# Optimization experiments

Measured on AMD Instinct MI355X. Metric: run time of the kernel, lower is better.

## Reference

```python
import jax, jax.numpy as jnp
import numpy as np

B, S, D, H = 4, 1024, 1024, 16
DK = D // H
MASK_WEIGHT_0 = 1.0   # weight for key-type 0 (from (weight, mask_mat) tuple)
MASK_WEIGHT_1 = 0.5   # weight for key-type 1
NEG_INF = -1.0e9


def setup_inputs() -> dict:
    key = jax.random.key(0)
    ks = jax.random.split(key, 10)
    wscale = 0.02
    return {
        "query": jax.random.normal(ks[0], (B, S, D), jnp.float32),
        "key_x": jax.random.normal(ks[1], (B, S, D), jnp.float32),
        "value": jax.random.normal(ks[2], (B, S, D), jnp.float32),
        "mask0": jax.random.randint(ks[3], (B, S, S), 0, 2, jnp.int32),
        "mask1": jax.random.randint(ks[4], (B, S, S), 0, 2, jnp.int32),
        "Wq":  wscale * jax.random.normal(ks[5], (D, D), jnp.float32),
        "Wk0": wscale * jax.random.normal(ks[6], (D, D), jnp.float32),
        "Wk1": wscale * jax.random.normal(ks[7], (D, D), jnp.float32),
        "Wv":  wscale * jax.random.normal(ks[8], (D, D), jnp.float32),
        "Wo":  wscale * jax.random.normal(ks[9], (D, D), jnp.float32),
    }


def _heads(x, W):
    # torch nn.Linear: x @ W.T ; then view(B,S,H,DK).transpose(1,2)
    return (x @ W.T).reshape(B, S, H, DK).transpose(0, 2, 1, 3)  # [B,H,S,DK]


def reference(query, key_x, value, mask0, mask1, Wq, Wk0, Wk1, Wv, Wo):
    q = _heads(query, Wq)          # [B,H,S,DK]
    k0 = _heads(key_x, Wk0)
    k1 = _heads(key_x, Wk1)
    v = _heads(value, Wv)
    scale = 1.0 / jnp.sqrt(jnp.float32(DK))

    def masked_score(k, mask, weight):
        s = jnp.einsum('bhqd,bhkd->bhqk', q, k) * scale       # [B,H,S,S]
        keep = (mask != 0)[:, None, :, :]                     # broadcast over heads
        # (score * weight*keep).masked_fill(mask==0, -1e9)
        return jnp.where(keep, s * weight, NEG_INF)

    scores = masked_score(k0, mask0, MASK_WEIGHT_0) + masked_score(k1, mask1, MASK_WEIGHT_1)
    p_attn = jax.nn.sigmoid(scores)                           # activation='sigmoid'
    x = jnp.einsum('bhqk,bhkd->bhqd', p_attn, v)              # [B,H,S,DK]
    x = x.transpose(0, 2, 1, 3).reshape(B, S, D)
    return x @ Wo.T                                            # output_linear (dropout p=0)
```

## Files before the change

kernel.cpp:

```cpp
#include <hip/hip_runtime.h>

#define B_  4
#define S_  1024
#define D_  1024
#define H_  16
#define DK_ 64

typedef __attribute__((ext_vector_type(8)))  short bf16x8;
typedef __attribute__((ext_vector_type(4)))  short bf16x4;
typedef __attribute__((ext_vector_type(4)))  float f32x4;
typedef __attribute__((ext_vector_type(16))) float f32x16;

static __device__ __forceinline__ unsigned short f2bf(float f) {
  union { float f; unsigned u; } v; v.f = f;
  unsigned r = v.u + 0x7FFFu + ((v.u >> 16) & 1u);
  return (unsigned short)(r >> 16);
}

static __device__ __forceinline__ unsigned cvtpk(float lo, float hi) {
  unsigned r;
  asm("v_cvt_pk_bf16_f32 %0, %1, %2" : "=v"(r) : "v"(lo), "v"(hi));
  return r;
}
static __device__ __forceinline__ void plswap(unsigned &a, unsigned &b) {
  asm volatile("v_permlane32_swap_b32 %0, %1" : "+v"(a), "+v"(b));
}

typedef __attribute__((address_space(1))) const void gc_t;
typedef __attribute__((address_space(3))) void lds_t;
static __device__ __forceinline__ void gload_lds16(const void* g, void* l) {
  __builtin_amdgcn_global_load_lds((gc_t*)g, (lds_t*)l, 16, 0, 0);
}

#define TM_ (1u << 22)
#define WM_ (1u << 20)

#define CEXP_ (-0.18033688011112042f)

__global__ __launch_bounds__(256)
void cvt_w(const float* __restrict__ w0, const float* __restrict__ w1,
           const float* __restrict__ w2, const float* __restrict__ w3,
           const float* __restrict__ w4, unsigned short* __restrict__ wbf)
{
  const size_t u = ((size_t)blockIdx.x * 256 + threadIdx.x) * 8;
  const int seg = (int)(u >> 20);
  const size_t off = u & (WM_ - 1);
  unsigned short t[8];
  if (seg == 1) {
    float4 a0 = *(const float4*)(w1 + off);
    float4 a1 = *(const float4*)(w1 + off + 4);
    float4 b0 = *(const float4*)(w2 + off);
    float4 b1 = *(const float4*)(w2 + off + 4);
    t[0]=f2bf(a0.x+0.5f*b0.x); t[1]=f2bf(a0.y+0.5f*b0.y);
    t[2]=f2bf(a0.z+0.5f*b0.z); t[3]=f2bf(a0.w+0.5f*b0.w);
    t[4]=f2bf(a1.x+0.5f*b1.x); t[5]=f2bf(a1.y+0.5f*b1.y);
    t[6]=f2bf(a1.z+0.5f*b1.z); t[7]=f2bf(a1.w+0.5f*b1.w);
  } else {
    const float sc = (seg == 0) ? CEXP_ : 1.0f;
    const float* src = (seg == 0) ? w0 : (seg == 2 ? w3 : w4);
    float4 f0 = *(const float4*)(src + off);
    float4 f1 = *(const float4*)(src + off + 4);
    t[0]=f2bf(sc*f0.x); t[1]=f2bf(sc*f0.y);
    t[2]=f2bf(sc*f0.z); t[3]=f2bf(sc*f0.w);
    t[4]=f2bf(sc*f1.x); t[5]=f2bf(sc*f1.y);
    t[6]=f2bf(sc*f1.z); t[7]=f2bf(sc*f1.w);
  }
  *(bf16x8*)(wbf + (size_t)seg * WM_ + off) = *(bf16x8*)t;
}

__global__ __launch_bounds__(256, 4)
void proj_gemm(const float* __restrict__ qx, const float* __restrict__ kx,
               const float* __restrict__ vx,
               const unsigned short* __restrict__ wbf,
               unsigned short* __restrict__ Qb, unsigned short* __restrict__ Kh,
               unsigned short* __restrict__ Vth,
               const int* __restrict__ ma, const int* __restrict__ mb,
               unsigned long long* __restrict__ pk)
{
  __shared__ unsigned short As[128][64];
  __shared__ unsigned short Ws[128][64];

  const int tid = threadIdx.x, bid = blockIdx.x;

  if (bid >= 768) {
    const int row = bid - 768;
    const int w4  = tid >> 6, lw = tid & 63;
    const int4 a  = *(const int4*)(ma + (size_t)row*1024 + w4*256 + lw*4);
    const int4 b  = *(const int4*)(mb + (size_t)row*1024 + w4*256 + lw*4);
    const unsigned long long b0 = __ballot((a.x != 0) & (b.x != 0));
    const unsigned long long b1 = __ballot((a.y != 0) & (b.y != 0));
    const unsigned long long b2 = __ballot((a.z != 0) & (b.z != 0));
    const unsigned long long b3 = __ballot((a.w != 0) & (b.w != 0));
    if (lw < 4) {
      const unsigned long long wv =
            ((b0 >> (16*lw)) & 0xFFFFull)
         | (((b1 >> (16*lw)) & 0xFFFFull) << 16)
         | (((b2 >> (16*lw)) & 0xFFFFull) << 32)
         | (((b3 >> (16*lw)) & 0xFFFFull) << 48);
      pk[(size_t)row*16 + w4*4 + lw] = wv;
    }
    return;
  }

  const int xcd = bid & 7, c = bid >> 3;
  const int L = xcd * 96 + c;
  const int which = L >> 8;
  const int rem = L & 255;
  const int mt = rem >> 3, nt = rem & 7;
  const int m0 = mt * 128, n0 = nt * 128;
  const int w = tid >> 6, l = tid & 63;
  const int lr = l & 15, lg = l >> 4;
  const int wr = w >> 1, wc = w & 1;

  const float* Af = (which == 0) ? qx : (which == 1) ? kx : vx;
  const unsigned short* W = wbf + (size_t)which * WM_;

  const f32x4 fzero = {0.f, 0.f, 0.f, 0.f};
  f32x4 acc[4][4];
#pragma unroll
  for (int m = 0; m < 4; m++)
#pragma unroll
    for (int n = 0; n < 4; n++) acc[m][n] = fzero;

  const int r0  = tid >> 3;
  const int cg  = tid & 7;
  const int aswz = (cg ^ (r0 & 7)) * 8;
  const float* aSrc = Af + (size_t)(m0 + r0) * 1024 + cg * 8;

  const int srow8 = l >> 3;
  const int sg    = ((l & 7) ^ srow8) * 8;
  const unsigned short* wBase = W + (size_t)(n0 + w*32 + srow8) * 1024 + sg;

  const int rc0 = ((lg)     ^ (lr & 7)) * 8;
  const int rc1 = ((4 + lg) ^ (lr & 7)) * 8;

  for (int kk = 0; kk < 1024; kk += 64) {
    float4 fa[4][2];
#pragma unroll
    for (int p = 0; p < 4; ++p) {
      const float* s = aSrc + (size_t)(p*32) * 1024 + kk;
      fa[p][0] = *(const float4*)s;
      fa[p][1] = *(const float4*)(s + 4);
    }
#pragma unroll
    for (int cc = 0; cc < 4; ++cc)
      gload_lds16(wBase + (size_t)cc * 8 * 1024 + kk, &Ws[w*32 + cc*8][0]);
#pragma unroll
    for (int p = 0; p < 4; ++p) {
      union { unsigned u[4]; bf16x8 v; } pu;
      pu.u[0] = cvtpk(fa[p][0].x, fa[p][0].y);
      pu.u[1] = cvtpk(fa[p][0].z, fa[p][0].w);
      pu.u[2] = cvtpk(fa[p][1].x, fa[p][1].y);
      pu.u[3] = cvtpk(fa[p][1].z, fa[p][1].w);
      *(bf16x8*)&As[p*32 + r0][aswz] = pu.v;
    }
    __syncthreads();

#pragma unroll
    for (int ks = 0; ks < 2; ++ks) {
      const int rc = ks ? rc1 : rc0;
      bf16x8 af[4], bfr[4];
#pragma unroll
      for (int m = 0; m < 4; m++) af[m]  = *(const bf16x8*)&As[wr*64 + m*16 + lr][rc];
#pragma unroll
      for (int n = 0; n < 4; n++) bfr[n] = *(const bf16x8*)&Ws[wc*64 + n*16 + lr][rc];
#pragma unroll
      for (int m = 0; m < 4; m++)
#pragma unroll
        for (int n = 0; n < 4; n++)
          acc[m][n] = __builtin_amdgcn_mfma_f32_16x16x32_bf16(af[m], bfr[n], acc[m][n], 0, 0, 0);
    }
    __syncthreads();
  }

  if (which == 2) {
#pragma unroll
    for (int m = 0; m < 4; m++) {
      const int row = m0 + wr*64 + m*16 + lg*4;
      const int b = row >> 10, s = row & 1023;
#pragma unroll
      for (int n = 0; n < 4; n++) {
        const int col = n0 + wc*64 + n*16 + lr;
        const int h = col >> 6, dk = col & 63;
        unsigned short tv[4] = {f2bf(acc[m][n][0]), f2bf(acc[m][n][1]),
                                f2bf(acc[m][n][2]), f2bf(acc[m][n][3])};
        const size_t a = ((size_t)((b*H_ + h)*DK_ + dk)) * S_
                       + (size_t)(s & ~63) + ((((s >> 3) & 7) ^ (dk & 7)) << 3) + (s & 7);
        *(bf16x4*)(Vth + a) = *(bf16x4*)tv;
      }
    }
  } else if (which == 0) {
#pragma unroll
    for (int m = 0; m < 4; m++) {
      const int row = m0 + wr*64 + m*16 + lg*4;
#pragma unroll
      for (int n = 0; n < 4; n++) {
        const int col = n0 + wc*64 + n*16 + lr;
#pragma unroll
        for (int r = 0; r < 4; r++)
          Qb[(size_t)(row + r) * 1024 + col] = f2bf(acc[m][n][r]);
      }
    }
  } else {
#pragma unroll
    for (int m = 0; m < 4; m++) {
      const int row = m0 + wr*64 + m*16 + lg*4;
#pragma unroll
      for (int n = 0; n < 4; n++) {
        const int col = n0 + wc*64 + n*16 + lr;
        const int h = col >> 6, dk = col & 63;
#pragma unroll
        for (int r = 0; r < 4; r++) {
          const int rr = row + r;
          const int b = rr >> 10, s = rr & 1023;
          const size_t a = ((size_t)((b*H_ + h)*S_ + s)) * 64
                         + (((dk >> 3) ^ (s & 7)) << 3) + (dk & 7);
          Kh[a] = f2bf(acc[m][n][r]);
        }
      }
    }
  }
}

__global__ __launch_bounds__(256, 4)
void out_gemm(const unsigned short* __restrict__ A,
              const unsigned short* __restrict__ W, float* __restrict__ C)
{
  __shared__ unsigned short As[128][64];
  __shared__ unsigned short Ws2[64][64];

  const int tid = threadIdx.x, bid = blockIdx.x;
  const int xcd = bid & 7, idx = bid >> 3;
  const int mt = (xcd << 2) | (idx & 3);
  const int nt = idx >> 2;
  const int m0 = mt * 128, n0 = nt * 64;
  const int w = tid >> 6, l = tid & 63;
  const int lr = l & 15, lg = l >> 4;
  const int wr = w >> 1, wc = w & 1;

  const f32x4 fzero = {0.f, 0.f, 0.f, 0.f};
  f32x4 acc[4][2];
#pragma unroll
  for (int m = 0; m < 4; m++)
#pragma unroll
    for (int n = 0; n < 2; n++) acc[m][n] = fzero;

  const int srow8 = l >> 3;
  const int sg    = ((l & 7) ^ srow8) * 8;
  const int rc0 = ((lg)     ^ (lr & 7)) * 8;
  const int rc1 = ((4 + lg) ^ (lr & 7)) * 8;

  const unsigned short* aBase = A + (size_t)(m0 + w*32 + srow8) * 1024 + sg;
  const unsigned short* wBase = W + (size_t)(n0 + w*16 + srow8) * 1024 + sg;

  for (int kk = 0; kk < 1024; kk += 64) {
#pragma unroll
    for (int cc = 0; cc < 4; ++cc)
      gload_lds16(aBase + (size_t)cc * 8 * 1024 + kk, &As[w*32 + cc*8][0]);
#pragma unroll
    for (int cc = 0; cc < 2; ++cc)
      gload_lds16(wBase + (size_t)cc * 8 * 1024 + kk, &Ws2[w*16 + cc*8][0]);
    __syncthreads();

#pragma unroll
    for (int ks = 0; ks < 2; ++ks) {
      const int rc = ks ? rc1 : rc0;
      bf16x8 af[4], bfr[2];
#pragma unroll
      for (int m = 0; m < 4; m++) af[m]  = *(const bf16x8*)&As[wr*64 + m*16 + lr][rc];
#pragma unroll
      for (int n = 0; n < 2; n++) bfr[n] = *(const bf16x8*)&Ws2[wc*32 + n*16 + lr][rc];
#pragma unroll
      for (int m = 0; m < 4; m++)
#pragma unroll
        for (int n = 0; n < 2; n++)
          acc[m][n] = __builtin_amdgcn_mfma_f32_16x16x32_bf16(af[m], bfr[n], acc[m][n], 0, 0, 0);
    }
    __syncthreads();
  }

#pragma unroll
  for (int m = 0; m < 4; m++) {
    const int row = m0 + wr*64 + m*16 + lg*4;
#pragma unroll
    for (int n = 0; n < 2; n++) {
      const int col = n0 + wc*32 + n*16 + lr;
#pragma unroll
      for (int r = 0; r < 4; r++)
        C[(size_t)(row + r) * 1024 + col] = acc[m][n][r];
    }
  }
}

__global__ __launch_bounds__(512)
void attn_kernel(const unsigned short* __restrict__ Q,
                 const unsigned short* __restrict__ Kh,
                 const unsigned short* __restrict__ Vth,
                 const unsigned long long* __restrict__ mpk,
                 unsigned short* __restrict__ X)
{
  __shared__ unsigned short Ks[2][2][4096];
  __shared__ unsigned short Vs[2][2][4096];

  const int tid  = threadIdx.x;
  const int bid0 = blockIdx.x;
  const int bid = ((bid0 & 7) << 6) | (bid0 >> 3);
  const int qt = bid & 7, h = (bid >> 3) & 15, b = bid >> 7;
  const int q0 = qt * 128;
  const int w8 = tid >> 6, lw = tid & 63;
  const int grp = w8 >> 2, qw = w8 & 3;
  const int l31 = lw & 31, hh = lw >> 5, l7 = lw & 7;
  const int bh = b * H_ + h;

  bf16x8 qf[4];
  {
    const unsigned short* qp = Q + ((size_t)(b*S_ + q0 + qw*32 + l31)) * D_ + h*DK_ + hh*8;
#pragma unroll
    for (int ds = 0; ds < 4; ++ds) qf[ds] = *(const bf16x8*)(qp + ds*16);
  }
  const size_t mbase = ((size_t)(b*S_ + q0 + qw*32 + l31)) * 16 + grp*8;

  f32x16 acc0, acc1;
#pragma unroll
  for (int r = 0; r < 16; ++r) { acc0[r] = 0.f; acc1[r] = 0.f; }

  const unsigned short* gp[4];
  unsigned short* lb[4];
  int stp[4];
#pragma unroll
  for (int c = 0; c < 4; ++c) {
    const int e = qw*4 + c;
    const int bu = e >> 3, s = e & 7;
    lb[c] = (bu == 0 ? &Ks[grp][0][0] : &Vs[grp][0][0]) + s*512;
    if (bu == 0) {
      gp[c]  = Kh + (size_t)bh * 65536 + grp*32768 + s*512 + lw*8;
      stp[c] = 4096;
    } else {
      gp[c]  = Vth + ((size_t)(bh*DK_ + s*8 + (lw >> 3))) * S_ + grp*512 + (lw & 7) * 8;
      stp[c] = 64;
    }
  }

#define STAGE(nxt)                                                     \
  {                                                                    \
    _Pragma("unroll")                                                  \
    for (int c = 0; c < 4; ++c) {                                      \
      gload_lds16(gp[c], lb[c] + (nxt)*4096);                          \
      gp[c] += stp[c];                                                 \
    }                                                                  \
  }

  STAGE(0);
  __syncthreads();
  unsigned long long mw = mpk[mbase];
  int cur = 0;

  for (int t = 0; t < 8; ++t) {
    unsigned long long mw_n = 0;
    if (t < 7) { STAGE(cur ^ 1); mw_n = mpk[mbase + t + 1]; }

#pragma unroll
    for (int sub = 0; sub < 2; ++sub) {
      const int rbase = (sub*32 + l31) * 64;
      f32x16 sv;
#pragma unroll
      for (int r = 0; r < 16; ++r) sv[r] = 0.f;
      __builtin_amdgcn_s_setprio(1);
#pragma unroll
      for (int ds = 0; ds < 4; ++ds) {
        const int g = (((ds*2 + hh) ^ l7)) * 8;
        const bf16x8 kf = *(const bf16x8*)&Ks[grp][cur][rbase + g];
        sv = __builtin_amdgcn_mfma_f32_32x32x16_bf16(kf, qf[ds], sv, 0, 0, 0);
      }
      __builtin_amdgcn_s_setprio(0);

      const unsigned long long ams = mw >> (8*sub + hh);
      float p[16];
#pragma unroll
      for (int r = 0; r < 16; ++r) {
        const int cbit = 16*(r & 3) + 2*(r >> 2);
        const float e  = __builtin_amdgcn_exp2f(sv[r]);
        const float pr = __builtin_amdgcn_rcpf(1.0f + e);
        p[r] = ((ams >> cbit) & 1ull) ? pr : 0.f;
      }

      bf16x8 pa[2];
#pragma unroll
      for (int ks = 0; ks < 2; ++ks) {
        const int a0 = ks*8;
        unsigned u0 = cvtpk(p[a0+0], p[a0+1]);
        unsigned u1 = cvtpk(p[a0+2], p[a0+3]);
        unsigned u2 = cvtpk(p[a0+4], p[a0+5]);
        unsigned u3 = cvtpk(p[a0+6], p[a0+7]);
        plswap(u0, u2);
        plswap(u1, u3);
        union { unsigned u[4]; bf16x8 v; } pu;
        pu.u[0] = u0; pu.u[1] = u1; pu.u[2] = u2; pu.u[3] = u3;
        pa[ks] = pu.v;
      }

      __builtin_amdgcn_s_setprio(1);
#pragma unroll
      for (int ks = 0; ks < 2; ++ks) {
        const int g = ((sub*4 + ks*2 + hh) ^ l7) * 8;
        const bf16x8 vb0 = *(const bf16x8*)&Vs[grp][cur][(l31)      * 64 + g];
        const bf16x8 vb1 = *(const bf16x8*)&Vs[grp][cur][(32 + l31) * 64 + g];
        acc0 = __builtin_amdgcn_mfma_f32_32x32x16_bf16(pa[ks], vb0, acc0, 0, 0, 0);
        acc1 = __builtin_amdgcn_mfma_f32_32x32x16_bf16(pa[ks], vb1, acc1, 0, 0, 0);
      }
      __builtin_amdgcn_s_setprio(0);
    }

    if (t < 7) {
      __syncthreads();
      mw = mw_n;
      cur ^= 1;
    }
  }
#undef STAGE

  __syncthreads();
  float2* cmb = (float2*)&Ks[0][0][0];
  if (grp == 1) {
#pragma unroll
    for (int i = 0; i < 8; ++i)
      cmb[(qw*16 + i)*64 + lw] = make_float2(acc0[2*i], acc0[2*i+1]);
#pragma unroll
    for (int i = 0; i < 8; ++i)
      cmb[(qw*16 + 8 + i)*64 + lw] = make_float2(acc1[2*i], acc1[2*i+1]);
  }
  __syncthreads();
  if (grp == 0) {
#pragma unroll
    for (int i = 0; i < 8; ++i) {
      float2 v = cmb[(qw*16 + i)*64 + lw];
      acc0[2*i] += v.x; acc0[2*i+1] += v.y;
    }
#pragma unroll
    for (int i = 0; i < 8; ++i) {
      float2 v = cmb[(qw*16 + 8 + i)*64 + lw];
      acc1[2*i] += v.x; acc1[2*i+1] += v.y;
    }
#pragma unroll
    for (int r = 0; r < 16; ++r) {
      const int qrow = q0 + qw*32 + (r & 3) + 8*(r >> 2) + 4*hh;
      unsigned short* xp = X + ((size_t)(b*S_ + qrow)) * D_ + h*DK_ + l31;
      xp[0]  = f2bf(acc0[r]);
      xp[32] = f2bf(acc1[r]);
    }
  }
}

extern "C" void kernel_launch(void* const* d_in, const int* in_sizes, int n_in,
                              void* d_out, int out_size, void* d_ws, size_t ws_size,
                              hipStream_t stream)
{
  const float* query = (const float*)d_in[0];
  const float* key_x = (const float*)d_in[1];
  const float* value = (const float*)d_in[2];
  const int*   mask0 = (const int*)d_in[3];
  const int*   mask1 = (const int*)d_in[4];
  const float* Wq    = (const float*)d_in[5];
  const float* Wk0   = (const float*)d_in[6];
  const float* Wk1   = (const float*)d_in[7];
  const float* Wv    = (const float*)d_in[8];
  const float* Wo    = (const float*)d_in[9];

  unsigned short* ws = (unsigned short*)d_ws;
  unsigned short* wbf = ws;
  unsigned short* Qb  = ws + (size_t)4 * WM_;
  unsigned short* Kh  = Qb  + (size_t)TM_;
  unsigned short* Vth = Kh  + (size_t)TM_;
  unsigned long long* mpk = (unsigned long long*)(Vth + (size_t)TM_);
  unsigned short* Xb = (unsigned short*)(mpk + 65536);

  cvt_w<<<dim3(2048), dim3(256), 0, stream>>>(Wq, Wk0, Wk1, Wv, Wo, wbf);

  proj_gemm<<<dim3(768 + 4096), dim3(256), 0, stream>>>(
      query, key_x, value, wbf, Qb, Kh, Vth, mask0, mask1, mpk);

  attn_kernel<<<dim3(B_ * H_ * (S_ / 128)), dim3(512), 0, stream>>>(
      Qb, Kh, Vth, mpk, Xb);

  out_gemm<<<dim3(512), dim3(256), 0, stream>>>(Xb, wbf + (size_t)3 * WM_,
                                                (float*)d_out);
}
```

Before: 94.42 us.

## Double-buffer projection GEMM LDS tiles with BK=32 software pipeline

```diff
diff --git a/kernel.cpp b/kernel.cpp
--- a/kernel.cpp
+++ b/kernel.cpp
@@ -77,8 +77,8 @@
                const int* __restrict__ ma, const int* __restrict__ mb,
                unsigned long long* __restrict__ pk)
 {
-  __shared__ unsigned short As[128][64];
-  __shared__ unsigned short Ws[128][64];
+  __shared__ unsigned short As[2][128][32];
+  __shared__ unsigned short Ws[2][128][32];
 
   const int tid = threadIdx.x, bid = blockIdx.x;
 
@@ -122,56 +122,58 @@
 #pragma unroll
     for (int n = 0; n < 4; n++) acc[m][n] = fzero;
 
-  const int r0  = tid >> 3;
-  const int cg  = tid & 7;
-  const int aswz = (cg ^ (r0 & 7)) * 8;
-  const float* aSrc = Af + (size_t)(m0 + r0) * 1024 + cg * 8;
-
-  const int srow8 = l >> 3;
-  const int sg    = ((l & 7) ^ srow8) * 8;
-  const unsigned short* wBase = W + (size_t)(n0 + w*32 + srow8) * 1024 + sg;
-
-  const int rc0 = ((lg)     ^ (lr & 7)) * 8;
-  const int rc1 = ((4 + lg) ^ (lr & 7)) * 8;
-
-  for (int kk = 0; kk < 1024; kk += 64) {
-    float4 fa[4][2];
-#pragma unroll
-    for (int p = 0; p < 4; ++p) {
-      const float* s = aSrc + (size_t)(p*32) * 1024 + kk;
-      fa[p][0] = *(const float4*)s;
-      fa[p][1] = *(const float4*)(s + 4);
-    }
-#pragma unroll
-    for (int cc = 0; cc < 4; ++cc)
-      gload_lds16(wBase + (size_t)cc * 8 * 1024 + kk, &Ws[w*32 + cc*8][0]);
-#pragma unroll
-    for (int p = 0; p < 4; ++p) {
-      union { unsigned u[4]; bf16x8 v; } pu;
-      pu.u[0] = cvtpk(fa[p][0].x, fa[p][0].y);
-      pu.u[1] = cvtpk(fa[p][0].z, fa[p][0].w);
-      pu.u[2] = cvtpk(fa[p][1].x, fa[p][1].y);
-      pu.u[3] = cvtpk(fa[p][1].z, fa[p][1].w);
-      *(bf16x8*)&As[p*32 + r0][aswz] = pu.v;
-    }
+  const int r0 = tid >> 1;
+  const int ch = (tid & 1) * 16;
+  const float* aSrc = Af + (size_t)(m0 + r0) * 1024 + ch;
+
+  const unsigned short* wBase = W + (size_t)(n0 + w*16 + (l >> 2)) * 1024 + (l & 3) * 8;
+
+  float4 fa[4];
+#define LOADA(kk)                                                        \
+  { fa[0] = *(const float4*)(aSrc + (kk));                               \
+    fa[1] = *(const float4*)(aSrc + (kk) + 4);                           \
+    fa[2] = *(const float4*)(aSrc + (kk) + 8);                           \
+    fa[3] = *(const float4*)(aSrc + (kk) + 12); }
+#define CVTWRITE(buf)                                                    \
+  { union { unsigned u[4]; bf16x8 v; } p0_, p1_;                         \
+    p0_.u[0] = cvtpk(fa[0].x, fa[0].y); p0_.u[1] = cvtpk(fa[0].z, fa[0].w); \
+    p0_.u[2] = cvtpk(fa[1].x, fa[1].y); p0_.u[3] = cvtpk(fa[1].z, fa[1].w); \
+    p1_.u[0] = cvtpk(fa[2].x, fa[2].y); p1_.u[1] = cvtpk(fa[2].z, fa[2].w); \
+    p1_.u[2] = cvtpk(fa[3].x, fa[3].y); p1_.u[3] = cvtpk(fa[3].z, fa[3].w); \
+    *(bf16x8*)&As[buf][r0][ch]     = p0_.v;                              \
+    *(bf16x8*)&As[buf][r0][ch + 8] = p1_.v; }
+#define LOADW(kk, buf)                                                   \
+  { gload_lds16(wBase + (kk),                     &Ws[buf][w*16][0]);    \
+    gload_lds16(wBase + (size_t)64*1024 + (kk),   &Ws[buf][w*16 + 64][0]); }
+
+  LOADA(0); CVTWRITE(0); LOADW(0, 0);
+  __syncthreads();
+  int cur = 0;
+
+  for (int t = 0; t < 32; ++t) {
+    const int kk1 = (t + 1) * 32;
+    if (t < 31) { LOADW(kk1, cur ^ 1); LOADA(kk1); }
+
+    __builtin_amdgcn_s_setprio(1);
+    bf16x8 af[4], bfr[4];
+#pragma unroll
+    for (int m = 0; m < 4; m++) af[m]  = *(const bf16x8*)&As[cur][wr*64 + m*16 + lr][lg*8];
+#pragma unroll
+    for (int n = 0; n < 4; n++) bfr[n] = *(const bf16x8*)&Ws[cur][wc*64 + n*16 + lr][lg*8];
+#pragma unroll
+    for (int m = 0; m < 4; m++)
+#pragma unroll
+      for (int n = 0; n < 4; n++)
+        acc[m][n] = __builtin_amdgcn_mfma_f32_16x16x32_bf16(af[m], bfr[n], acc[m][n], 0, 0, 0);
+    __builtin_amdgcn_s_setprio(0);
+
+    if (t < 31) CVTWRITE(cur ^ 1);
     __syncthreads();
-
-#pragma unroll
-    for (int ks = 0; ks < 2; ++ks) {
-      const int rc = ks ? rc1 : rc0;
-      bf16x8 af[4], bfr[4];
-#pragma unroll
-      for (int m = 0; m < 4; m++) af[m]  = *(const bf16x8*)&As[wr*64 + m*16 + lr][rc];
-#pragma unroll
-      for (int n = 0; n < 4; n++) bfr[n] = *(const bf16x8*)&Ws[wc*64 + n*16 + lr][rc];
-#pragma unroll
-      for (int m = 0; m < 4; m++)
-#pragma unroll
-        for (int n = 0; n < 4; n++)
-          acc[m][n] = __builtin_amdgcn_mfma_f32_16x16x32_bf16(af[m], bfr[n], acc[m][n], 0, 0, 0);
-    }
-    __syncthreads();
-  }
+    cur ^= 1;
+  }
+#undef LOADA
+#undef CVTWRITE
+#undef LOADW
 
   if (which == 2) {
 #pragma unroll
```

After: 103.3 us. +9.4%, slower.
